# Performance work log

Hardware: AMD Instinct MI355X
Metric: run time of the kernel (lower is better)

Reference implementation:

```python
import jax, jax.numpy as jnp
import numpy as np

B, S, T = 64, 256, 64
E, H = 256, 256
VS, VT = 32000, 32000


def _lstm_cell(x, h, c, Wih, Whh, b):
    # torch gate order: i, f, g, o
    g = x @ Wih.T + h @ Whh.T + b
    i, f, gg, o = jnp.split(g, 4, axis=-1)
    i = jax.nn.sigmoid(i); f = jax.nn.sigmoid(f); o = jax.nn.sigmoid(o)
    gg = jnp.tanh(gg)
    c2 = f * c + i * gg
    h2 = o * jnp.tanh(c2)
    return h2, c2


def _run_lstm(xs, h0, c0, Wih, Whh, b, reverse=False):
    # xs: [S, B, in]
    def step(carry, x):
        h, c = carry
        h2, c2 = _lstm_cell(x, h, c, Wih, Whh, b)
        return (h2, c2), h2
    (hT, cT), ys = jax.lax.scan(step, (h0, c0), xs, reverse=reverse)
    return ys, hT, cT


def setup_inputs():
    key = jax.random.key(0)
    ks = jax.random.split(key, 24)
    sc = 0.05
    rn = lambda k, shp: (jax.random.normal(k, shp, jnp.float32) * sc)
    inp = {
        'src': jax.random.randint(ks[0], (B, S), 0, VS, jnp.int32),
        'tgt_input': jax.random.randint(ks[1], (B, T), 0, VT, jnp.int32),
        'src_emb': rn(ks[2], (VS, E)).at[0].set(0.0),   # padding_idx=0
        'tgt_emb': rn(ks[3], (VT, E)).at[0].set(0.0),
        'enc_f_Wih': rn(ks[4], (4 * H, E)), 'enc_f_Whh': rn(ks[5], (4 * H, H)), 'enc_f_b': rn(ks[6], (4 * H,)),
        'enc_b_Wih': rn(ks[7], (4 * H, E)), 'enc_b_Whh': rn(ks[8], (4 * H, H)), 'enc_b_b': rn(ks[9], (4 * H,)),
        # decoder layer0 input = embed (E) + context (2H)
        'dec0_Wih': rn(ks[10], (4 * H, E + 2 * H)), 'dec0_Whh': rn(ks[11], (4 * H, H)), 'dec0_b': rn(ks[12], (4 * H,)),
        'dec1_Wih': rn(ks[13], (4 * H, H)), 'dec1_Whh': rn(ks[14], (4 * H, H)), 'dec1_b': rn(ks[15], (4 * H,)),
        'attn_W': rn(ks[16], (H, 3 * H)), 'attn_b': rn(ks[17], (H,)),
        'attn_v': jax.random.uniform(ks[18], (H,), jnp.float32),
        'proj_W': rn(ks[19], (VT, H)), 'proj_b': rn(ks[20], (VT,)),
    }
    return inp


def reference(src, tgt_input, src_emb, tgt_emb,
              enc_f_Wih, enc_f_Whh, enc_f_b, enc_b_Wih, enc_b_Whh, enc_b_b,
              dec0_Wih, dec0_Whh, dec0_b, dec1_Wih, dec1_Whh, dec1_b,
              attn_W, attn_b, attn_v, proj_W, proj_b):
    b = src.shape[0]
    zeros = jnp.zeros((b, H), jnp.float32)

    # ---- encoder (1-layer bidirectional LSTM), eval-mode (no dropout) ----
    xs = src_emb[src].transpose(1, 0, 2)  # [S, B, E]
    ys_f, hf, cf = _run_lstm(xs, zeros, zeros, enc_f_Wih, enc_f_Whh, enc_f_b, reverse=False)
    ys_b, hb, cb = _run_lstm(xs, zeros, zeros, enc_b_Wih, enc_b_Whh, enc_b_b, reverse=True)
    enc_out = jnp.concatenate([ys_f, ys_b], axis=-1).transpose(1, 0, 2)  # [B, S, 2H]

    # combined fwd+bwd states, repeated across both decoder layers
    h_init = hf + hb  # [B, H]
    c_init = cf + cb

    # ---- attention precompute: encoder part of attn Linear ----
    Wa_h = attn_W[:, :H]        # applied to decoder hidden
    Wa_e = attn_W[:, H:]        # applied to encoder_outputs
    enc_proj = jnp.einsum('bsd,hd->bsh', enc_out, Wa_e) + attn_b  # [B, S, H]

    # ---- decoder: per-step attention + 2-layer LSTM ----
    tgt_e = tgt_emb[tgt_input].transpose(1, 0, 2)  # [T, B, E]

    def dec_step(carry, emb_t):
        h0, c0, h1, c1 = carry
        # Bahdanau attention on top-layer hidden h1
        energy = jnp.tanh(h1 @ Wa_h.T[..., None, :] if False else
                          jnp.tanh(0.0))  # placeholder never used
        e = jnp.tanh(enc_proj + (h1 @ Wa_h.T)[:, None, :])  # [B, S, H]
        score = jnp.einsum('bsh,h->bs', e, attn_v)
        a = jax.nn.softmax(score, axis=1)
        ctx = jnp.einsum('bs,bsd->bd', a, enc_out)  # [B, 2H]
        x = jnp.concatenate([emb_t, ctx], axis=-1)  # [B, E+2H]
        h0n, c0n = _lstm_cell(x, h0, c0, dec0_Wih, dec0_Whh, dec0_b)
        h1n, c1n = _lstm_cell(h0n, h1, c1, dec1_Wih, dec1_Whh, dec1_b)
        return (h0n, c0n, h1n, c1n), h1n

    _, outs = jax.lax.scan(dec_step, (h_init, c_init, h_init, c_init), tgt_e)
    dec_out = outs.transpose(1, 0, 2)  # [B, T, H]
    logits = dec_out @ proj_W.T + proj_b  # [B, T, VT]
    return logits
```

## Files before the change

### kernel.cpp

```cpp
#include <hip/hip_runtime.h>

typedef unsigned short u16;
typedef unsigned int u32;
typedef unsigned long long u64;
typedef short s8v __attribute__((ext_vector_type(8)));
typedef float f32x4 __attribute__((ext_vector_type(4)));
typedef unsigned short us4 __attribute__((ext_vector_type(4)));

#define MFMA16(a,b,c) __builtin_amdgcn_mfma_f32_16x16x32_bf16(a,b,c,0,0,0)

__device__ __forceinline__ float b2f(u16 u){ union{u32 i; float f;} v; v.i=((u32)u)<<16; return v.f; }
__device__ __forceinline__ u16 f2b(float f){ union{float f; u32 i;} v; v.f=f; u32 r=v.i+0x7FFFu+((v.i>>16)&1u); return (u16)(r>>16); }
__device__ __forceinline__ float sigf(float x){ return 1.f/(1.f+__expf(-x)); }
__device__ __forceinline__ float tanh_(float x){ x=fminf(15.f,fmaxf(-15.f,x)); float e=__expf(2.f*x); return (e-1.f)/(e+1.f); }
__device__ __forceinline__ float tanhs(float x){ float e=__expf(2.f*x); return 1.f - 2.f/(e+1.f); }

union FU { s8v v; us4 h[2]; };

__device__ __forceinline__ us4 ld8_sys(const u16* p){
  u64 v = __hip_atomic_load((const u64*)p, __ATOMIC_RELAXED, __HIP_MEMORY_SCOPE_AGENT);
  union{u64 q; us4 h;} x; x.q=v; return x.h;
}
__device__ __forceinline__ float2 ld8f2(const float* p){
  u64 v = __hip_atomic_load((const u64*)p, __ATOMIC_RELAXED, __HIP_MEMORY_SCOPE_AGENT);
  union{u64 q; float2 f;} x; x.q=v; return x.f;
}
__device__ __forceinline__ void st4_sys(u16* p, u32 v){
  __hip_atomic_store((u32*)p, v, __ATOMIC_RELAXED, __HIP_MEMORY_SCOPE_AGENT);
}
__device__ __forceinline__ void st4f(float* p, float v){
  union{float f; u32 i;} u; u.f=v;
  __hip_atomic_store((u32*)p, u.i, __ATOMIC_RELAXED, __HIP_MEMORY_SCOPE_AGENT);
}
__device__ __forceinline__ void st8_sys(u16* p, us4 v){
  union{us4 h; u64 q;} x; x.h=v;
  __hip_atomic_store((u64*)p, x.q, __ATOMIC_RELAXED, __HIP_MEMORY_SCOPE_AGENT);
}
__device__ __forceinline__ int ldcnt(const int* p){
  return __hip_atomic_load(p, __ATOMIC_RELAXED, __HIP_MEMORY_SCOPE_AGENT);
}
__device__ __forceinline__ void addcnt(int* p){
  __hip_atomic_fetch_add(p, 1, __ATOMIC_RELAXED, __HIP_MEMORY_SCOPE_AGENT);
}

__device__ __forceinline__ s8v gfrag(const u16* rowp, int kbase, int g4){
  FU u; const u16* p = rowp + kbase + 4*g4;
  u.h[0] = *(const us4*)p; u.h[1] = *(const us4*)(p+16);
  return u.v;
}
__device__ __forceinline__ s8v ldsfrag(const u16* lds, int ldk, int row, int kbase, int g4){
  int sw = row&7;
  int g0 = ((kbase+4*g4)>>2)^sw, g1 = ((kbase+16+4*g4)>>2)^sw;
  FU u;
  u.h[0] = *(const us4*)&lds[row*ldk + (g0<<2)];
  u.h[1] = *(const us4*)&lds[row*ldk + (g1<<2)];
  return u.v;
}

__global__ __launch_bounds__(256) void prep_kernel(
    const float* Wihf, const float* Whhf, const float* Wihb, const float* Whhb,
    const float* d0Wih, const float* d0Whh, const float* d1Wih, const float* d1Whh,
    const float* attnW, const float* projW,
    u16* oWihf, u16* oWhhf, u16* oWihb, u16* oWhhb,
    u16* oW0, u16* oW1, u16* oWaH, u16* oWaE, u16* oprojW){
  long long i = (long long)blockIdx.x*256 + threadIdx.x;
  const long long N1 = 262144;
  if (i < N1){ oWihf[i] = f2b(Wihf[i]); return; } i -= N1;
  if (i < N1){ oWhhf[i] = f2b(Whhf[i]); return; } i -= N1;
  if (i < N1){ oWihb[i] = f2b(Wihb[i]); return; } i -= N1;
  if (i < N1){ oWhhb[i] = f2b(Whhb[i]); return; } i -= N1;
  if (i < 1048576){
    int g = (int)(i>>10), k = (int)(i&1023);
    float v = (k<768) ? d0Wih[(size_t)g*768+k] : d0Whh[(size_t)g*256 + (k-768)];
    oW0[i] = f2b(v); return;
  } i -= 1048576;
  if (i < 524288){
    int g = (int)(i>>9), k = (int)(i&511);
    float v = (k<256) ? d1Wih[(size_t)g*256+k] : d1Whh[(size_t)g*256 + (k-256)];
    oW1[i] = f2b(v); return;
  } i -= 524288;
  if (i < 65536){ int n=(int)(i>>8), k=(int)(i&255); oWaH[i] = f2b(attnW[(size_t)n*768+k]); return; } i -= 65536;
  if (i < 131072){ int n=(int)(i>>9), k=(int)(i&511); oWaE[i] = f2b(attnW[(size_t)n*768+256+k]); return; } i -= 131072;
  if (i < 8192000){ oprojW[i] = f2b(projW[i]); return; }
}

__global__ __launch_bounds__(256) void gather_kernel(
    const int* src, const int* tgt, const float* src_emb, const float* tgt_emb,
    u16* xs, u16* temb){
  long long i = (long long)blockIdx.x*256 + threadIdx.x;
  if (i < 4194304){
    int e = (int)(i&255); int sb = (int)(i>>8);
    int s = sb>>6, b = sb&63;
    int idx = src[b*256 + s];
    xs[i] = f2b(src_emb[(size_t)idx*256 + e]);
    return;
  }
  long long j = i - 4194304;
  if (j < 1048576){
    int e = (int)(j&255); int tb = (int)(j>>8);
    int t = tb>>6, b = tb&63;
    int idx = tgt[b*64 + t];
    temb[j] = f2b(tgt_emb[(size_t)idx*256 + e]);
  }
}

template<int K, int OBF>
__global__ __launch_bounds__(256) void gemm64(
    const u16* __restrict__ A, int lda, const u16* __restrict__ Bw, int ldb,
    const float* __restrict__ bias, void* Cout, long long ldc){
  __shared__ u16 Alds[64*K];
  int tid = threadIdx.x;
  long long mt = blockIdx.x, nt = blockIdx.y;
  const int Kc8 = K>>3;
  for (int it = tid; it < 64*Kc8; it += 256){
    int row = it / Kc8, seg = it % Kc8;
    const u16* src = A + (size_t)(mt*64+row)*lda + seg*8;
    us4 a0 = *(const us4*)src, a1 = *(const us4*)(src+4);
    int sw = row&7;
    *(us4*)&Alds[row*K + ((((seg*2  ))^sw)<<2)] = a0;
    *(us4*)&Alds[row*K + ((((seg*2+1))^sw)<<2)] = a1;
  }
  __syncthreads();
  int w = tid>>6, lane = tid&63;
  int l15 = lane&15, g4 = lane>>4;
  int arow = w*16 + l15;
  const int NKT = K>>5;
  s8v af[NKT];
  #pragma unroll
  for (int kt=0; kt<NKT; ++kt) af[kt] = ldsfrag(Alds, K, arow, kt*32, g4);
  f32x4 acc[4];
  #pragma unroll
  for (int nti=0; nti<4; ++nti){
    const u16* brow = Bw + (size_t)(nt*64 + nti*16 + l15)*ldb;
    f32x4 a = {0.f,0.f,0.f,0.f};
    #pragma unroll
    for (int kt=0; kt<NKT; ++kt) a = MFMA16(af[kt], gfrag(brow, kt*32, g4), a);
    acc[nti] = a;
  }
  #pragma unroll
  for (int nti=0; nti<4; ++nti)
    #pragma unroll
    for (int r=0; r<4; ++r){
      long long rowg = mt*64 + w*16 + 4*g4 + r;
      long long colg = nt*64 + nti*16 + l15;
      float v = acc[nti][r] + bias[colg];
      if (OBF) ((u16*)Cout)[rowg*ldc + colg] = f2b(v);
      else     ((float*)Cout)[rowg*ldc + colg] = v;
    }
}

__global__ __launch_bounds__(512,2) void encoder_kernel(
    const u16* __restrict__ XWf, const u16* __restrict__ XWb,
    const u16* __restrict__ Whhf, const u16* __restrict__ Whhb,
    u16* __restrict__ enc_out, float* hTf, float* cTf, float* hTb, float* cTb,
    u16* hx, int* ecnt){
  int bid = blockIdx.x, tid = threadIdx.x;
  int dir = bid&1, bb=(bid>>1)&3, ch=bid>>3;
  const u16* XW  = dir ? XWb : XWf;
  const u16* Whh = dir ? Whhb : Whhf;
  float* hT = dir ? hTb : hTf; float* cT = dir ? cTb : cTf;
  int w = tid>>6, lane = tid&63, l15=lane&15, g4=lane>>4;
  int bg0 = bb*16;
  s8v bwf[4][8];
  #pragma unroll
  for (int i=0;i<4;++i){
    int t4 = w*4+i, q=t4>>3, jt=t4&7;
    const u16* wr = Whh + (size_t)(q*256 + ch*128 + jt*16 + l15)*256;
    #pragma unroll
    for (int kt=0;kt<8;++kt) bwf[i][kt] = gfrag(wr, kt*32, g4);
  }
  int gb = tid>>5, cl = (tid&31)*4;
  float cst[4]={0.f,0.f,0.f,0.f};
  __shared__ u16 hbuf[16*256];
  __shared__ float gacc[512][17];
  for (int i=tid;i<4096;i+=512) hbuf[i]=0;
  __syncthreads();
  int* myc = &ecnt[bid*32];
  int* pc  = &ecnt[(bid^8)*32];
  u16* myhx = hx + (size_t)bid*2*16*128;
  const u16* phx = hx + (size_t)(bid^8)*2*16*128;
  for (int t=0;t<256;++t){
    int s = dir ? 255-t : t;
    us4 xw4[4];
    const u16* xwr = XW + (((size_t)s*64 + bg0 + gb))*1024 + ch*128 + cl;
    #pragma unroll
    for (int qq=0;qq<4;++qq) xw4[qq] = *(const us4*)(xwr + qq*256);
    s8v af[8];
    #pragma unroll
    for (int kt=0;kt<8;++kt) af[kt] = ldsfrag(hbuf, 256, l15, kt*32, g4);
    #pragma unroll
    for (int i=0;i<4;++i){
      f32x4 a={0.f,0.f,0.f,0.f};
      #pragma unroll
      for (int kt=0;kt<8;++kt) a = MFMA16(af[kt], bwf[i][kt], a);
      int t4=w*4+i, q=t4>>3, jt=t4&7;
      #pragma unroll
      for (int r=0;r<4;++r) gacc[q*128 + jt*16 + l15][4*g4+r] = a[r];
    }
    __syncthreads();
    float hvv[4];
    #pragma unroll
    for (int cc=0;cc<4;++cc){
      int clc = cl+cc;
      float gi = gacc[clc][gb]     + b2f(xw4[0][cc]);
      float gf = gacc[128+clc][gb] + b2f(xw4[1][cc]);
      float gg = gacc[256+clc][gb] + b2f(xw4[2][cc]);
      float go = gacc[384+clc][gb] + b2f(xw4[3][cc]);
      float iv=sigf(gi), fv=sigf(gf), gv=tanh_(gg), ov=sigf(go);
      float cn = fv*cst[cc]+iv*gv; cst[cc]=cn;
      hvv[cc] = ov*tanh_(cn);
    }
    us4 hv4;
    #pragma unroll
    for (int cc=0;cc<4;++cc) hv4[cc] = f2b(hvv[cc]);
    *(us4*)&enc_out[(((size_t)(bg0+gb)*256 + s))*512 + dir*256 + ch*128 + cl] = hv4;
    if (t==255){
      #pragma unroll
      for (int cc=0;cc<4;++cc){
        hT[(bg0+gb)*256 + ch*128 + cl+cc] = hvv[cc];
        cT[(bg0+gb)*256 + ch*128 + cl+cc] = cst[cc];
      }
    } else {
      int col = ch*128 + cl;
      *(us4*)&hbuf[gb*256 + ((((col>>2)) ^ (gb&7))<<2)] = hv4;
      st8_sys(myhx + ((size_t)(t&1)*16*128) + gb*128 + cl, hv4);
      asm volatile("s_waitcnt vmcnt(0)" ::: "memory");
      __syncthreads();
      if (tid==0){
        addcnt(myc);
        while (ldcnt(pc) < t+1) __builtin_amdgcn_s_sleep(1);
      }
      __syncthreads();
      int b2 = tid>>5, cl4 = (tid&31)*4;
      us4 pv = ld8_sys(phx + ((size_t)(t&1)*16*128) + b2*128 + cl4);
      int pcol = (1-ch)*128 + cl4;
      *(us4*)&hbuf[b2*256 + ((((pcol>>2)) ^ (b2&7))<<2)] = pv;
      __syncthreads();
    }
  }
}

__global__ __launch_bounds__(256) void init_states(
    const float* hTf, const float* hTb, const float* cTf, const float* cTb,
    float* c0g, float* c1g, u16* h0buf, u16* h1buf){
  int i = blockIdx.x*256 + threadIdx.x;
  float h = hTf[i] + hTb[i];
  float c = cTf[i] + cTb[i];
  c0g[i]=c; c1g[i]=c;
  u16 hb = f2b(h);
  h0buf[16384+i] = hb;
  h1buf[16384+i] = hb;
}

__global__ __launch_bounds__(512,2) void decoder_kernel(
    const u16* __restrict__ epb, const u16* __restrict__ enc, const u16* __restrict__ temb,
    const u16* __restrict__ WaH, const u16* __restrict__ W0, const u16* __restrict__ W1,
    const float* __restrict__ attn_v, const float* __restrict__ b0, const float* __restrict__ b1,
    const float* __restrict__ c0init, const float* __restrict__ c1init,
    u16* h0buf, u16* h1buf, u16* ctxg, float* scoreg, u16* dout, int* dcnt){
  int bid = blockIdx.x, tid = threadIdx.x;
  int c = bid&15, g = bid>>4;
  int w = tid>>6, lane = tid&63, l15 = lane&15, g4 = lane>>4;
  int bg0 = g*8;
  int q = w&3, kh = w>>2;
  const u16* w0r = W0 + (size_t)(q*256 + c*16 + l15)*1024 + kh*512;
  const u16* w1r = W1 + (size_t)(q*256 + c*16 + l15)*512  + kh*256;
  u32 encp[64];
  {
    int dp = lane&15, sq = lane>>4;
    const u16* eb2 = enc + ((size_t)((bg0+w)*256 + sq*64))*512 + c*32 + dp*2;
    #pragma unroll
    for (int sl=0; sl<64; ++sl) encp[sl] = *(const u32*)(eb2 + (size_t)sl*512);
  }
  int cb = tid>>4, ci = tid&15;
  float c0r=0.f, c1r=0.f, bias0[4], bias1[4];
  if (tid<128){
    c0r = c0init[(bg0+cb)*256 + c*16+ci];
    c1r = c1init[(bg0+cb)*256 + c*16+ci];
    #pragma unroll
    for (int qq=0;qq<4;++qq){ bias0[qq]=b0[qq*256 + c*16+ci]; bias1[qq]=b1[qq*256 + c*16+ci]; }
  }
  __shared__ u16 epl[128*264];
  __shared__ u16 x0l[16*1024];
  __shared__ u16 x1l[16*512];
  __shared__ u16 h1l[16*256];
  __shared__ float qls[8][257];
  __shared__ float scls[8][257];
  __shared__ float red[8][16][17];
  __shared__ float vl[256];
  if (tid<256) vl[tid] = attn_v[tid];
  for (int i=tid;i<8192;i+=512) x0l[8192+i]=0;
  for (int i=tid;i<4096;i+=512) x1l[4096+i]=0;
  for (int i=tid;i<2048;i+=512) h1l[2048+i]=0;
  {
    int pr = tid>>2, k2 = tid&3;
    int b2 = pr>>4, sl = pr&15;
    const u16* ep = epb + ((size_t)((bg0+b2)*256 + c*16+sl))*256 + k2*64;
    u16* dst = &epl[(b2*16+sl)*264 + k2*66];
    #pragma unroll
    for (int u2=0; u2<16; ++u2){
      us4 v4 = *(const us4*)(ep + u2*4);
      *(u32*)&dst[u2*4]   = (u32)(u16)v4[0] | ((u32)(u16)v4[1]<<16);
      *(u32*)&dst[u2*4+2] = (u32)(u16)v4[2] | ((u32)(u16)v4[3]<<16);
    }
  }
  __syncthreads();
  int* cnt = &dcnt[g*32];
  int bt = 0;

#define GBAR() do{ bt += 16; \
    asm volatile("s_waitcnt vmcnt(0)" ::: "memory"); \
    __syncthreads(); \
    if (tid==0){ addcnt(cnt); while (ldcnt(cnt) < bt) __builtin_amdgcn_s_sleep(1); } \
    __syncthreads(); }while(0)

  for (int tt=0; tt<64; ++tt){
    int par = tt&1, pp = par^1;
    {
      int b2 = tid>>6, c4 = lane*4;
      us4 hv4 = ld8_sys(h1buf + (size_t)pp*16384 + (bg0+b2)*256 + c4);
      *(us4*)&h1l[b2*256 + ((((c4>>2)) ^ b2)<<2)] = hv4;
      int col = 256 + c4;
      *(us4*)&x1l[b2*512 + ((((col>>2)) ^ b2)<<2)] = hv4;
    }
    __syncthreads();
    #pragma unroll
    for (int t2=0;t2<2;++t2){
      int ct = w*2+t2;
      const u16* br = WaH + (size_t)(ct*16 + l15)*256;
      f32x4 a = {0.f,0.f,0.f,0.f};
      #pragma unroll
      for (int kt=0;kt<8;++kt) a = MFMA16(ldsfrag(h1l,256,l15,kt*32,g4), gfrag(br,kt*32,g4), a);
      #pragma unroll
      for (int r=0;r<4;++r){ int row=4*g4+r; if(row<8) qls[row][ct*16+l15] = a[r]; }
    }
    __syncthreads();
    {
      int pr = tid>>2, k2 = tid&3;
      int b2 = pr>>4, sl = pr&15, s = c*16+sl;
      const u16* base2 = &epl[(b2*16+sl)*264 + k2*66];
      float p = 0.f;
      #pragma unroll 8
      for (int u2=0; u2<32; ++u2){
        u32 e2 = *(const u32*)&base2[u2*2];
        int h = k2*64 + u2*2;
        p += tanhs(b2f((u16)(e2&0xFFFFu)) + qls[b2][h])   * vl[h];
        p += tanhs(b2f((u16)(e2>>16))     + qls[b2][h+1]) * vl[h+1];
      }
      p += __shfl_xor(p,1); p += __shfl_xor(p,2);
      if (k2==0) st4f(scoreg + (size_t)(bg0+b2)*256 + s, p);
    }
    GBAR();
    #pragma unroll
    for (int k=0;k<2;++k){
      int idx = tid + k*512;
      int b2 = idx>>7, s2 = (idx&127)*2;
      float2 f2 = ld8f2(scoreg + (size_t)(bg0+b2)*256 + s2);
      scls[b2][s2] = f2.x; scls[b2][s2+1] = f2.y;
    }
    __syncthreads();
    {
      int b2 = w;
      float a0=scls[b2][lane*4], a1=scls[b2][lane*4+1], a2=scls[b2][lane*4+2], a3=scls[b2][lane*4+3];
      float m = fmaxf(fmaxf(a0,a1),fmaxf(a2,a3));
      #pragma unroll
      for (int o2=32;o2;o2>>=1) m = fmaxf(m, __shfl_xor(m,o2));
      float e0=__expf(a0-m), e1=__expf(a1-m), e2=__expf(a2-m), e3=__expf(a3-m);
      float sm = e0+e1+e2+e3;
      #pragma unroll
      for (int o2=32;o2;o2>>=1) sm += __shfl_xor(sm,o2);
      float inv = 1.f/sm;
      scls[b2][lane*4]=e0*inv; scls[b2][lane*4+1]=e1*inv; scls[b2][lane*4+2]=e2*inv; scls[b2][lane*4+3]=e3*inv;
    }
    __syncthreads();
    {
      int dp = lane&15, sq = lane>>4, b2 = w;
      float cp0=0.f, cp1=0.f;
      #pragma unroll
      for (int sl=0; sl<64; ++sl){
        float wgt = scls[b2][sq*64+sl];
        u32 e2 = encp[sl];
        cp0 += wgt * b2f((u16)(e2&0xFFFFu));
        cp1 += wgt * b2f((u16)(e2>>16));
      }
      cp0 += __shfl_xor(cp0,16); cp0 += __shfl_xor(cp0,32);
      cp1 += __shfl_xor(cp1,16); cp1 += __shfl_xor(cp1,32);
      if (sq==0){
        u32 pk = (u32)f2b(cp0) | ((u32)f2b(cp1)<<16);
        st4_sys(ctxg + (size_t)(bg0+b2)*512 + c*32 + dp*2, pk);
      }
    }
    GBAR();
    {
      int b2 = tid>>6, e4 = lane*4;
      us4 tv = *(const us4*)(temb + ((size_t)tt*64 + bg0 + b2)*256 + e4);
      *(us4*)&x0l[b2*1024 + ((((e4>>2)) ^ b2)<<2)] = tv;
    }
    #pragma unroll
    for (int k=0;k<2;++k){
      int idx = tid + k*512;
      int b2 = idx>>7, c4 = (idx&127)*4;
      us4 cv = ld8_sys(ctxg + (size_t)(bg0+b2)*512 + c4);
      int col = 256 + c4;
      *(us4*)&x0l[b2*1024 + ((((col>>2)) ^ b2)<<2)] = cv;
    }
    {
      int b2 = tid>>6, c4 = lane*4;
      us4 hv4 = ld8_sys(h0buf + (size_t)pp*16384 + (bg0+b2)*256 + c4);
      int col = 768 + c4;
      *(us4*)&x0l[b2*1024 + ((((col>>2)) ^ b2)<<2)] = hv4;
    }
    __syncthreads();
    {
      f32x4 a={0.f,0.f,0.f,0.f};
      #pragma unroll
      for (int kt=0;kt<16;++kt)
        a = MFMA16(ldsfrag(x0l,1024,l15,kh*512+kt*32,g4), gfrag(w0r, kt*32, g4), a);
      #pragma unroll
      for (int r=0;r<4;++r) red[w][4*g4+r][l15] = a[r];
    }
    __syncthreads();
    if (tid<128){
      float gi = red[0][cb][ci]+red[4][cb][ci]+bias0[0];
      float gf = red[1][cb][ci]+red[5][cb][ci]+bias0[1];
      float gg = red[2][cb][ci]+red[6][cb][ci]+bias0[2];
      float go = red[3][cb][ci]+red[7][cb][ci]+bias0[3];
      float iv=sigf(gi), fv=sigf(gf), gv=tanh_(gg), ov=sigf(go);
      float cn = fv*c0r+iv*gv; c0r=cn;
      float hv = ov*tanh_(cn);
      int me=f2b(hv), ot=__shfl_xor(me,1);
      if ((tid&1)==0) st4_sys(h0buf + (size_t)par*16384 + (bg0+cb)*256 + c*16+ci,
                              ((u32)me&0xFFFFu)|((u32)ot<<16));
    }
    GBAR();
    {
      int b2 = tid>>6, c4 = lane*4;
      us4 hv4 = ld8_sys(h0buf + (size_t)par*16384 + (bg0+b2)*256 + c4);
      *(us4*)&x1l[b2*512 + ((((c4>>2)) ^ b2)<<2)] = hv4;
    }
    __syncthreads();
    {
      f32x4 a={0.f,0.f,0.f,0.f};
      #pragma unroll
      for (int kt=0;kt<8;++kt)
        a = MFMA16(ldsfrag(x1l,512,l15,kh*256+kt*32,g4), gfrag(w1r, kt*32, g4), a);
      #pragma unroll
      for (int r=0;r<4;++r) red[w][4*g4+r][l15] = a[r];
    }
    __syncthreads();
    if (tid<128){
      float gi = red[0][cb][ci]+red[4][cb][ci]+bias1[0];
      float gf = red[1][cb][ci]+red[5][cb][ci]+bias1[1];
      float gg = red[2][cb][ci]+red[6][cb][ci]+bias1[2];
      float go = red[3][cb][ci]+red[7][cb][ci]+bias1[3];
      float iv=sigf(gi), fv=sigf(gf), gv=tanh_(gg), ov=sigf(go);
      float cn = fv*c1r+iv*gv; c1r=cn;
      float hv = ov*tanh_(cn);
      int me=f2b(hv), ot=__shfl_xor(me,1);
      if ((tid&1)==0){
        u32 pk = ((u32)me&0xFFFFu)|((u32)ot<<16);
        st4_sys(h1buf + (size_t)par*16384 + (bg0+cb)*256 + c*16+ci, pk);
        *(u32*)&dout[((size_t)(bg0+cb)*64+tt)*256 + c*16+ci] = pk;
      }
    }
    GBAR();
  }
#undef GBAR
}

extern "C" void kernel_launch(void* const* d_in, const int* in_sizes, int n_in,
                              void* d_out, int out_size, void* d_ws, size_t ws_size,
                              hipStream_t stream){
  const int*   src     = (const int*)  d_in[0];
  const int*   tgt     = (const int*)  d_in[1];
  const float* src_emb = (const float*)d_in[2];
  const float* tgt_emb = (const float*)d_in[3];
  const float* encfWih = (const float*)d_in[4];
  const float* encfWhh = (const float*)d_in[5];
  const float* encfb   = (const float*)d_in[6];
  const float* encbWih = (const float*)d_in[7];
  const float* encbWhh = (const float*)d_in[8];
  const float* encbb   = (const float*)d_in[9];
  const float* d0Wih   = (const float*)d_in[10];
  const float* d0Whh   = (const float*)d_in[11];
  const float* d0b     = (const float*)d_in[12];
  const float* d1Wih   = (const float*)d_in[13];
  const float* d1Whh   = (const float*)d_in[14];
  const float* d1b     = (const float*)d_in[15];
  const float* attnW   = (const float*)d_in[16];
  const float* attnb   = (const float*)d_in[17];
  const float* attnv   = (const float*)d_in[18];
  const float* projW   = (const float*)d_in[19];
  const float* projb   = (const float*)d_in[20];

  char* ws = (char*)d_ws;
  size_t off = 0;
  auto alloc = [&](size_t bytes)->char*{ char* p = ws + off; off += (bytes + 255) & ~(size_t)255; return p; };

  int* dcnt     = (int*)alloc(1024);
  int* ecnt     = (int*)alloc(2048);
  u16* xs       = (u16*)alloc(16384ULL*256*2);
  u16* temb     = (u16*)alloc(4096ULL*256*2);
  u16* oWihf    = (u16*)alloc(262144ULL*2);
  u16* oWhhf    = (u16*)alloc(262144ULL*2);
  u16* oWihb    = (u16*)alloc(262144ULL*2);
  u16* oWhhb    = (u16*)alloc(262144ULL*2);
  u16* oW0      = (u16*)alloc(1048576ULL*2);
  u16* oW1      = (u16*)alloc(524288ULL*2);
  u16* oWaH     = (u16*)alloc(65536ULL*2);
  u16* oWaE     = (u16*)alloc(131072ULL*2);
  u16* oprojW   = (u16*)alloc(8192000ULL*2);
  u16* XWf      = (u16*)alloc(16384ULL*1024*2);
  u16* XWb      = (u16*)alloc(16384ULL*1024*2);
  u16* enc      = (u16*)alloc(64ULL*256*512*2);
  u16* epb      = (u16*)alloc(64ULL*256*256*2);
  float* hTf    = (float*)alloc(16384ULL*4);
  float* cTf    = (float*)alloc(16384ULL*4);
  float* hTb    = (float*)alloc(16384ULL*4);
  float* cTb    = (float*)alloc(16384ULL*4);
  float* c0g    = (float*)alloc(16384ULL*4);
  float* c1g    = (float*)alloc(16384ULL*4);
  u16* h0buf    = (u16*)alloc(2ULL*16384*2);
  u16* h1buf    = (u16*)alloc(2ULL*16384*2);
  u16* ctxg     = (u16*)alloc(64ULL*512*2);
  float* scoreg = (float*)alloc(16384ULL*4);
  u16* hx       = (u16*)alloc(16ULL*2*16*128*2);
  u16* dout     = (u16*)alloc(4096ULL*256*2);
  if (off > ws_size) return;

  hipMemsetAsync(dcnt, 0, 1024, stream);
  hipMemsetAsync(ecnt, 0, 2048, stream);

  prep_kernel<<<43008, 256, 0, stream>>>(encfWih, encfWhh, encbWih, encbWhh,
      d0Wih, d0Whh, d1Wih, d1Whh, attnW, projW,
      oWihf, oWhhf, oWihb, oWhhb, oW0, oW1, oWaH, oWaE, oprojW);

  gather_kernel<<<20480, 256, 0, stream>>>(src, tgt, src_emb, tgt_emb, xs, temb);

  gemm64<256,1><<<dim3(256,16), 256, 0, stream>>>(xs, 256, oWihf, 256, encfb, XWf, 1024);
  gemm64<256,1><<<dim3(256,16), 256, 0, stream>>>(xs, 256, oWihb, 256, encbb, XWb, 1024);

  encoder_kernel<<<16, 512, 0, stream>>>(XWf, XWb, oWhhf, oWhhb, enc, hTf, cTf, hTb, cTb, hx, ecnt);

  gemm64<512,1><<<dim3(256,4), 256, 0, stream>>>(enc, 512, oWaE, 512, attnb, epb, 256);

  init_states<<<64, 256, 0, stream>>>(hTf, hTb, cTf, cTb, c0g, c1g, h0buf, h1buf);

  decoder_kernel<<<128, 512, 0, stream>>>(epb, enc, temb, oWaH, oW0, oW1,
      attnv, d0b, d1b, c0g, c1g, h0buf, h1buf, ctxg, scoreg, dout, dcnt);

  gemm64<256,0><<<dim3(64,500), 256, 0, stream>>>(dout, 256, oprojW, 256, projb, (float*)d_out, 32000);
}
```

Before: 4.728 ms.

## Use per-block flag barrier in decoder and stream encoder Whh from memory

The decoder's group barrier switches from a shared atomic counter (one fetch_add per block, then polling) to per-block flags on separate cache lines. Each block stores its epoch, and one wavefront polls all 16 flags in parallel and min-reduces them with shuffles, which removes atomic contention on a single counter. Separately, the encoder no longer keeps the Whh fragments in registers; it reloads them from global or L2 memory each timestep. This frees a large number of registers but adds memory traffic on the serial recurrence path.

```diff
diff --git a/kernel.cpp b/kernel.cpp
--- a/kernel.cpp
+++ b/kernel.cpp
@@ -38,6 +38,9 @@
 }
 __device__ __forceinline__ int ldcnt(const int* p){
   return __hip_atomic_load(p, __ATOMIC_RELAXED, __HIP_MEMORY_SCOPE_AGENT);
+}
+__device__ __forceinline__ void stcnt(int* p, int v){
+  __hip_atomic_store(p, v, __ATOMIC_RELAXED, __HIP_MEMORY_SCOPE_AGENT);
 }
 __device__ __forceinline__ void addcnt(int* p){
   __hip_atomic_fetch_add(p, 1, __ATOMIC_RELAXED, __HIP_MEMORY_SCOPE_AGENT);
@@ -161,13 +164,11 @@
   float* hT = dir ? hTb : hTf; float* cT = dir ? cTb : cTf;
   int w = tid>>6, lane = tid&63, l15=lane&15, g4=lane>>4;
   int bg0 = bb*16;
-  s8v bwf[4][8];
+  const u16* wrp[4];
   #pragma unroll
   for (int i=0;i<4;++i){
     int t4 = w*4+i, q=t4>>3, jt=t4&7;
-    const u16* wr = Whh + (size_t)(q*256 + ch*128 + jt*16 + l15)*256;
-    #pragma unroll
-    for (int kt=0;kt<8;++kt) bwf[i][kt] = gfrag(wr, kt*32, g4);
+    wrp[i] = Whh + (size_t)(q*256 + ch*128 + jt*16 + l15)*256;
   }
   int gb = tid>>5, cl = (tid&31)*4;
   float cst[4]={0.f,0.f,0.f,0.f};
@@ -192,7 +193,7 @@
     for (int i=0;i<4;++i){
       f32x4 a={0.f,0.f,0.f,0.f};
       #pragma unroll
-      for (int kt=0;kt<8;++kt) a = MFMA16(af[kt], bwf[i][kt], a);
+      for (int kt=0;kt<8;++kt) a = MFMA16(af[kt], gfrag(wrp[i], kt*32, g4), a);
       int t4=w*4+i, q=t4>>3, jt=t4&7;
       #pragma unroll
       for (int r=0;r<4;++r) gacc[q*128 + jt*16 + l15][4*g4+r] = a[r];
@@ -257,7 +258,7 @@
     const u16* __restrict__ WaH, const u16* __restrict__ W0, const u16* __restrict__ W1,
     const float* __restrict__ attn_v, const float* __restrict__ b0, const float* __restrict__ b1,
     const float* __restrict__ c0init, const float* __restrict__ c1init,
-    u16* h0buf, u16* h1buf, u16* ctxg, float* scoreg, u16* dout, int* dcnt){
+    u16* h0buf, u16* h1buf, u16* ctxg, float* scoreg, u16* dout, int* dflag){
   int bid = blockIdx.x, tid = threadIdx.x;
   int c = bid&15, g = bid>>4;
   int w = tid>>6, lane = tid&63, l15 = lane&15, g4 = lane>>4;
@@ -305,13 +306,25 @@
     }
   }
   __syncthreads();
-  int* cnt = &dcnt[g*32];
+  int* myflag = &dflag[(g*16 + c)*64];
+  int* gflags = &dflag[g*16*64];
   int bt = 0;
 
-#define GBAR() do{ bt += 16; \
+#define GBAR() do{ bt += 1; \
     asm volatile("s_waitcnt vmcnt(0)" ::: "memory"); \
     __syncthreads(); \
-    if (tid==0){ addcnt(cnt); while (ldcnt(cnt) < bt) __builtin_amdgcn_s_sleep(1); } \
+    if (tid==0) stcnt(myflag, bt); \
+    if (tid<64){ \
+      int v_; \
+      do{ __builtin_amdgcn_s_sleep(1); \
+          v_ = ldcnt(&gflags[(lane&15)*64]); \
+          int m_; \
+          m_ = __shfl_xor(v_,1); v_ = v_<m_?v_:m_; \
+          m_ = __shfl_xor(v_,2); v_ = v_<m_?v_:m_; \
+          m_ = __shfl_xor(v_,4); v_ = v_<m_?v_:m_; \
+          m_ = __shfl_xor(v_,8); v_ = v_<m_?v_:m_; \
+      } while (v_ < bt); \
+    } \
     __syncthreads(); }while(0)
 
   for (int tt=0; tt<64; ++tt){
@@ -497,7 +510,7 @@
   size_t off = 0;
   auto alloc = [&](size_t bytes)->char*{ char* p = ws + off; off += (bytes + 255) & ~(size_t)255; return p; };
 
-  int* dcnt     = (int*)alloc(1024);
+  int* dflag    = (int*)alloc(32768);
   int* ecnt     = (int*)alloc(2048);
   u16* xs       = (u16*)alloc(16384ULL*256*2);
   u16* temb     = (u16*)alloc(4096ULL*256*2);
@@ -528,7 +541,7 @@
   u16* dout     = (u16*)alloc(4096ULL*256*2);
   if (off > ws_size) return;
 
-  hipMemsetAsync(dcnt, 0, 1024, stream);
+  hipMemsetAsync(dflag, 0, 32768, stream);
   hipMemsetAsync(ecnt, 0, 2048, stream);
 
   prep_kernel<<<43008, 256, 0, stream>>>(encfWih, encfWhh, encbWih, encbWhh,
@@ -547,7 +560,7 @@
   init_states<<<64, 256, 0, stream>>>(hTf, hTb, cTf, cTb, c0g, c1g, h0buf, h1buf);
 
   decoder_kernel<<<128, 512, 0, stream>>>(epb, enc, temb, oWaH, oW0, oW1,
-      attnv, d0b, d1b, c0g, c1g, h0buf, h1buf, ctxg, scoreg, dout, dcnt);
+      attnv, d0b, d1b, c0g, c1g, h0buf, h1buf, ctxg, scoreg, dout, dflag);
 
   gemm64<256,0><<<dim3(64,500), 256, 0, stream>>>(dout, 256, oprojW, 256, projb, (float*)d_out, 32000);
 }
```

After: 4.717 ms. About the same (-0.2%).

## Decoder: one block per batch row, drop grid barriers; encoder streams Whh

Applied to the files above, without the earlier changes.

The decoder is restructured from 128 cooperating blocks that synchronised through global-memory counters into 64 independent 1024-thread blocks, each owning a single batch row for all timesteps. This removes the per-step grid barriers and the global round trips for scores, context and hidden states. The cost is much worse MFMA utilisation: only one row of each 16-row tile is non-zero, so every block re-reads the full W0/W1/WaH weights from global or L2 on each step. The encoder also stops keeping Whh fragments in registers and reloads them from global memory every timestep, which lowers register pressure but adds memory traffic.

```diff
diff --git a/kernel.cpp b/kernel.cpp
--- a/kernel.cpp
+++ b/kernel.cpp
@@ -20,17 +20,6 @@
 __device__ __forceinline__ us4 ld8_sys(const u16* p){
   u64 v = __hip_atomic_load((const u64*)p, __ATOMIC_RELAXED, __HIP_MEMORY_SCOPE_AGENT);
   union{u64 q; us4 h;} x; x.q=v; return x.h;
-}
-__device__ __forceinline__ float2 ld8f2(const float* p){
-  u64 v = __hip_atomic_load((const u64*)p, __ATOMIC_RELAXED, __HIP_MEMORY_SCOPE_AGENT);
-  union{u64 q; float2 f;} x; x.q=v; return x.f;
-}
-__device__ __forceinline__ void st4_sys(u16* p, u32 v){
-  __hip_atomic_store((u32*)p, v, __ATOMIC_RELAXED, __HIP_MEMORY_SCOPE_AGENT);
-}
-__device__ __forceinline__ void st4f(float* p, float v){
-  union{float f; u32 i;} u; u.f=v;
-  __hip_atomic_store((u32*)p, u.i, __ATOMIC_RELAXED, __HIP_MEMORY_SCOPE_AGENT);
 }
 __device__ __forceinline__ void st8_sys(u16* p, us4 v){
   union{us4 h; u64 q;} x; x.h=v;
@@ -161,13 +150,11 @@
   float* hT = dir ? hTb : hTf; float* cT = dir ? cTb : cTf;
   int w = tid>>6, lane = tid&63, l15=lane&15, g4=lane>>4;
   int bg0 = bb*16;
-  s8v bwf[4][8];
+  const u16* wrp[4];
   #pragma unroll
   for (int i=0;i<4;++i){
     int t4 = w*4+i, q=t4>>3, jt=t4&7;
-    const u16* wr = Whh + (size_t)(q*256 + ch*128 + jt*16 + l15)*256;
-    #pragma unroll
-    for (int kt=0;kt<8;++kt) bwf[i][kt] = gfrag(wr, kt*32, g4);
+    wrp[i] = Whh + (size_t)(q*256 + ch*128 + jt*16 + l15)*256;
   }
   int gb = tid>>5, cl = (tid&31)*4;
   float cst[4]={0.f,0.f,0.f,0.f};
@@ -192,7 +179,7 @@
     for (int i=0;i<4;++i){
       f32x4 a={0.f,0.f,0.f,0.f};
       #pragma unroll
-      for (int kt=0;kt<8;++kt) a = MFMA16(af[kt], bwf[i][kt], a);
+      for (int kt=0;kt<8;++kt) a = MFMA16(af[kt], gfrag(wrp[i], kt*32, g4), a);
       int t4=w*4+i, q=t4>>3, jt=t4&7;
       #pragma unroll
       for (int r=0;r<4;++r) gacc[q*128 + jt*16 + l15][4*g4+r] = a[r];
@@ -252,51 +239,31 @@
   h1buf[16384+i] = hb;
 }
 
-__global__ __launch_bounds__(512,2) void decoder_kernel(
+__global__ __launch_bounds__(1024,1) void decoder_kernel(
     const u16* __restrict__ epb, const u16* __restrict__ enc, const u16* __restrict__ temb,
     const u16* __restrict__ WaH, const u16* __restrict__ W0, const u16* __restrict__ W1,
     const float* __restrict__ attn_v, const float* __restrict__ b0, const float* __restrict__ b1,
     const float* __restrict__ c0init, const float* __restrict__ c1init,
-    u16* h0buf, u16* h1buf, u16* ctxg, float* scoreg, u16* dout, int* dcnt){
-  int bid = blockIdx.x, tid = threadIdx.x;
-  int c = bid&15, g = bid>>4;
-  int w = tid>>6, lane = tid&63, l15 = lane&15, g4 = lane>>4;
-  int bg0 = g*8;
-  int q = w&3, kh = w>>2;
-  const u16* w0r = W0 + (size_t)(q*256 + c*16 + l15)*1024 + kh*512;
-  const u16* w1r = W1 + (size_t)(q*256 + c*16 + l15)*512  + kh*256;
-  u32 encp[64];
+    const u16* __restrict__ hinit, u16* __restrict__ dout){
+  int b = blockIdx.x, tid = threadIdx.x;
+  int wv = tid>>6, lane = tid&63, l15 = lane&15, g4 = lane>>4;
+  __shared__ u16 epl[256*264];
+  __shared__ float part[4][512];
+  __shared__ float qls[256];
+  __shared__ float scs[256];
+  __shared__ float af2[256];
+  __shared__ float vl[256];
+  __shared__ float gacc[1024];
+  __shared__ float c0l[256];
+  __shared__ float c1l[256];
+  __shared__ u16 x0l[1024];
+  __shared__ u16 x1l[512];
+  __shared__ u16 h0l[256];
+  __shared__ u16 h1l[256];
   {
-    int dp = lane&15, sq = lane>>4;
-    const u16* eb2 = enc + ((size_t)((bg0+w)*256 + sq*64))*512 + c*32 + dp*2;
-    #pragma unroll
-    for (int sl=0; sl<64; ++sl) encp[sl] = *(const u32*)(eb2 + (size_t)sl*512);
-  }
-  int cb = tid>>4, ci = tid&15;
-  float c0r=0.f, c1r=0.f, bias0[4], bias1[4];
-  if (tid<128){
-    c0r = c0init[(bg0+cb)*256 + c*16+ci];
-    c1r = c1init[(bg0+cb)*256 + c*16+ci];
-    #pragma unroll
-    for (int qq=0;qq<4;++qq){ bias0[qq]=b0[qq*256 + c*16+ci]; bias1[qq]=b1[qq*256 + c*16+ci]; }
-  }
-  __shared__ u16 epl[128*264];
-  __shared__ u16 x0l[16*1024];
-  __shared__ u16 x1l[16*512];
-  __shared__ u16 h1l[16*256];
-  __shared__ float qls[8][257];
-  __shared__ float scls[8][257];
-  __shared__ float red[8][16][17];
-  __shared__ float vl[256];
-  if (tid<256) vl[tid] = attn_v[tid];
-  for (int i=tid;i<8192;i+=512) x0l[8192+i]=0;
-  for (int i=tid;i<4096;i+=512) x1l[4096+i]=0;
-  for (int i=tid;i<2048;i+=512) h1l[2048+i]=0;
-  {
-    int pr = tid>>2, k2 = tid&3;
-    int b2 = pr>>4, sl = pr&15;
-    const u16* ep = epb + ((size_t)((bg0+b2)*256 + c*16+sl))*256 + k2*64;
-    u16* dst = &epl[(b2*16+sl)*264 + k2*66];
+    int s = tid>>2, k2 = tid&3;
+    const u16* ep = epb + ((size_t)(b*256 + s))*256 + k2*64;
+    u16* dst = &epl[s*264 + k2*66];
     #pragma unroll
     for (int u2=0; u2<16; ++u2){
       us4 v4 = *(const us4*)(ep + u2*4);
@@ -304,64 +271,48 @@
       *(u32*)&dst[u2*4+2] = (u32)(u16)v4[2] | ((u32)(u16)v4[3]<<16);
     }
   }
+  if (tid<256){
+    vl[tid] = attn_v[tid];
+    u16 h = hinit[b*256+tid];
+    h1l[tid] = h; h0l[tid] = h;
+    c0l[tid] = c0init[b*256+tid];
+    c1l[tid] = c1init[b*256+tid];
+  }
   __syncthreads();
-  int* cnt = &dcnt[g*32];
-  int bt = 0;
-
-#define GBAR() do{ bt += 16; \
-    asm volatile("s_waitcnt vmcnt(0)" ::: "memory"); \
-    __syncthreads(); \
-    if (tid==0){ addcnt(cnt); while (ldcnt(cnt) < bt) __builtin_amdgcn_s_sleep(1); } \
-    __syncthreads(); }while(0)
-
+  const s8v zf = {0,0,0,0,0,0,0,0};
   for (int tt=0; tt<64; ++tt){
-    int par = tt&1, pp = par^1;
     {
-      int b2 = tid>>6, c4 = lane*4;
-      us4 hv4 = ld8_sys(h1buf + (size_t)pp*16384 + (bg0+b2)*256 + c4);
-      *(us4*)&h1l[b2*256 + ((((c4>>2)) ^ b2)<<2)] = hv4;
-      int col = 256 + c4;
-      *(us4*)&x1l[b2*512 + ((((col>>2)) ^ b2)<<2)] = hv4;
-    }
-    __syncthreads();
-    #pragma unroll
-    for (int t2=0;t2<2;++t2){
-      int ct = w*2+t2;
-      const u16* br = WaH + (size_t)(ct*16 + l15)*256;
-      f32x4 a = {0.f,0.f,0.f,0.f};
-      #pragma unroll
-      for (int kt=0;kt<8;++kt) a = MFMA16(ldsfrag(h1l,256,l15,kt*32,g4), gfrag(br,kt*32,g4), a);
-      #pragma unroll
-      for (int r=0;r<4;++r){ int row=4*g4+r; if(row<8) qls[row][ct*16+l15] = a[r]; }
+      int h = tid>>2, k2 = tid&3;
+      const u16* wr = WaH + (size_t)h*256 + k2*64;
+      float qv = 0.f;
+      #pragma unroll 4
+      for (int u2=0; u2<16; ++u2){
+        us4 w4 = *(const us4*)(wr + u2*4);
+        int k = k2*64 + u2*4;
+        qv += b2f(w4[0])*b2f(h1l[k])   + b2f(w4[1])*b2f(h1l[k+1])
+            + b2f(w4[2])*b2f(h1l[k+2]) + b2f(w4[3])*b2f(h1l[k+3]);
+      }
+      qv += __shfl_xor(qv,1); qv += __shfl_xor(qv,2);
+      if (k2==0) qls[h] = qv;
     }
     __syncthreads();
     {
-      int pr = tid>>2, k2 = tid&3;
-      int b2 = pr>>4, sl = pr&15, s = c*16+sl;
-      const u16* base2 = &epl[(b2*16+sl)*264 + k2*66];
+      int s = tid>>2, k2 = tid&3;
+      const u16* base2 = &epl[s*264 + k2*66];
       float p = 0.f;
       #pragma unroll 8
       for (int u2=0; u2<32; ++u2){
         u32 e2 = *(const u32*)&base2[u2*2];
         int h = k2*64 + u2*2;
-        p += tanhs(b2f((u16)(e2&0xFFFFu)) + qls[b2][h])   * vl[h];
-        p += tanhs(b2f((u16)(e2>>16))     + qls[b2][h+1]) * vl[h+1];
+        p += tanhs(b2f((u16)(e2&0xFFFFu)) + qls[h])   * vl[h];
+        p += tanhs(b2f((u16)(e2>>16))     + qls[h+1]) * vl[h+1];
       }
       p += __shfl_xor(p,1); p += __shfl_xor(p,2);
-      if (k2==0) st4f(scoreg + (size_t)(bg0+b2)*256 + s, p);
-    }
-    GBAR();
-    #pragma unroll
-    for (int k=0;k<2;++k){
-      int idx = tid + k*512;
-      int b2 = idx>>7, s2 = (idx&127)*2;
-      float2 f2 = ld8f2(scoreg + (size_t)(bg0+b2)*256 + s2);
-      scls[b2][s2] = f2.x; scls[b2][s2+1] = f2.y;
-    }
-    __syncthreads();
-    {
-      int b2 = w;
-      float a0=scls[b2][lane*4], a1=scls[b2][lane*4+1], a2=scls[b2][lane*4+2], a3=scls[b2][lane*4+3];
+      if (k2==0) scs[s] = p;
+    }
+    __syncthreads();
+    if (wv==0){
+      float a0=scs[lane*4],a1=scs[lane*4+1],a2=scs[lane*4+2],a3=scs[lane*4+3];
       float m = fmaxf(fmaxf(a0,a1),fmaxf(a2,a3));
       #pragma unroll
       for (int o2=32;o2;o2>>=1) m = fmaxf(m, __shfl_xor(m,o2));
@@ -370,102 +321,106 @@
       #pragma unroll
       for (int o2=32;o2;o2>>=1) sm += __shfl_xor(sm,o2);
       float inv = 1.f/sm;
-      scls[b2][lane*4]=e0*inv; scls[b2][lane*4+1]=e1*inv; scls[b2][lane*4+2]=e2*inv; scls[b2][lane*4+3]=e3*inv;
+      af2[lane*4]=e0*inv; af2[lane*4+1]=e1*inv; af2[lane*4+2]=e2*inv; af2[lane*4+3]=e3*inv;
     }
     __syncthreads();
     {
-      int dp = lane&15, sq = lane>>4, b2 = w;
+      int soff = tid>>8, dp = tid&255;
+      const u16* ebase = enc + ((size_t)b*256)*512 + dp*2;
       float cp0=0.f, cp1=0.f;
-      #pragma unroll
-      for (int sl=0; sl<64; ++sl){
-        float wgt = scls[b2][sq*64+sl];
-        u32 e2 = encp[sl];
+      #pragma unroll 8
+      for (int ck=0; ck<64; ++ck){
+        int s = ck*4 + soff;
+        u32 e2 = *(const u32*)(ebase + (size_t)s*512);
+        float wgt = af2[s];
         cp0 += wgt * b2f((u16)(e2&0xFFFFu));
         cp1 += wgt * b2f((u16)(e2>>16));
       }
-      cp0 += __shfl_xor(cp0,16); cp0 += __shfl_xor(cp0,32);
-      cp1 += __shfl_xor(cp1,16); cp1 += __shfl_xor(cp1,32);
-      if (sq==0){
-        u32 pk = (u32)f2b(cp0) | ((u32)f2b(cp1)<<16);
-        st4_sys(ctxg + (size_t)(bg0+b2)*512 + c*32 + dp*2, pk);
-      }
-    }
-    GBAR();
+      part[soff][dp*2] = cp0; part[soff][dp*2+1] = cp1;
+    }
+    __syncthreads();
+    if (tid<512){
+      float cx = part[0][tid]+part[1][tid]+part[2][tid]+part[3][tid];
+      x0l[256+tid] = f2b(cx);
+    } else if (tid<768){
+      int j = tid-512;
+      x0l[j] = temb[((size_t)tt*64 + b)*256 + j];
+    } else {
+      int j = tid-768;
+      x0l[768+j] = h0l[j];
+    }
+    __syncthreads();
     {
-      int b2 = tid>>6, e4 = lane*4;
-      us4 tv = *(const us4*)(temb + ((size_t)tt*64 + bg0 + b2)*256 + e4);
-      *(us4*)&x0l[b2*1024 + ((((e4>>2)) ^ b2)<<2)] = tv;
-    }
-    #pragma unroll
-    for (int k=0;k<2;++k){
-      int idx = tid + k*512;
-      int b2 = idx>>7, c4 = (idx&127)*4;
-      us4 cv = ld8_sys(ctxg + (size_t)(bg0+b2)*512 + c4);
-      int col = 256 + c4;
-      *(us4*)&x0l[b2*1024 + ((((col>>2)) ^ b2)<<2)] = cv;
-    }
+      f32x4 acc0={0.f,0.f,0.f,0.f},acc1={0.f,0.f,0.f,0.f},acc2={0.f,0.f,0.f,0.f},acc3={0.f,0.f,0.f,0.f};
+      const u16* wbase = W0 + (size_t)(wv*64 + l15)*1024;
+      for (int kt=0; kt<32; ++kt){
+        s8v af = zf;
+        if (l15==0){
+          FU u; u.h[0] = *(const us4*)&x0l[kt*32+4*g4]; u.h[1] = *(const us4*)&x0l[kt*32+4*g4+16];
+          af = u.v;
+        }
+        acc0 = MFMA16(af, gfrag(wbase,           kt*32, g4), acc0);
+        acc1 = MFMA16(af, gfrag(wbase + 16*1024, kt*32, g4), acc1);
+        acc2 = MFMA16(af, gfrag(wbase + 32*1024, kt*32, g4), acc2);
+        acc3 = MFMA16(af, gfrag(wbase + 48*1024, kt*32, g4), acc3);
+      }
+      if (g4==0){
+        gacc[wv*64 + l15]      = acc0[0];
+        gacc[wv*64 + 16 + l15] = acc1[0];
+        gacc[wv*64 + 32 + l15] = acc2[0];
+        gacc[wv*64 + 48 + l15] = acc3[0];
+      }
+    }
+    __syncthreads();
+    if (tid<256){
+      float iv = sigf(gacc[tid]      + b0[tid]);
+      float fv = sigf(gacc[256+tid]  + b0[256+tid]);
+      float gv = tanh_(gacc[512+tid] + b0[512+tid]);
+      float ov = sigf(gacc[768+tid]  + b0[768+tid]);
+      float cn = fv*c0l[tid] + iv*gv; c0l[tid] = cn;
+      float hv = ov*tanh_(cn);
+      u16 hb = f2b(hv);
+      h0l[tid] = hb;
+      x1l[tid] = hb;
+    } else if (tid<512){
+      x1l[tid] = h1l[tid-256];
+    }
+    __syncthreads();
     {
-      int b2 = tid>>6, c4 = lane*4;
-      us4 hv4 = ld8_sys(h0buf + (size_t)pp*16384 + (bg0+b2)*256 + c4);
-      int col = 768 + c4;
-      *(us4*)&x0l[b2*1024 + ((((col>>2)) ^ b2)<<2)] = hv4;
-    }
-    __syncthreads();
-    {
-      f32x4 a={0.f,0.f,0.f,0.f};
-      #pragma unroll
-      for (int kt=0;kt<16;++kt)
-        a = MFMA16(ldsfrag(x0l,1024,l15,kh*512+kt*32,g4), gfrag(w0r, kt*32, g4), a);
-      #pragma unroll
-      for (int r=0;r<4;++r) red[w][4*g4+r][l15] = a[r];
-    }
-    __syncthreads();
-    if (tid<128){
-      float gi = red[0][cb][ci]+red[4][cb][ci]+bias0[0];
-      float gf = red[1][cb][ci]+red[5][cb][ci]+bias0[1];
-      float gg = red[2][cb][ci]+red[6][cb][ci]+bias0[2];
-      float go = red[3][cb][ci]+red[7][cb][ci]+bias0[3];
-      float iv=sigf(gi), fv=sigf(gf), gv=tanh_(gg), ov=sigf(go);
-      float cn = fv*c0r+iv*gv; c0r=cn;
+      f32x4 acc0={0.f,0.f,0.f,0.f},acc1={0.f,0.f,0.f,0.f},acc2={0.f,0.f,0.f,0.f},acc3={0.f,0.f,0.f,0.f};
+      const u16* wbase = W1 + (size_t)(wv*64 + l15)*512;
+      for (int kt=0; kt<16; ++kt){
+        s8v af = zf;
+        if (l15==0){
+          FU u; u.h[0] = *(const us4*)&x1l[kt*32+4*g4]; u.h[1] = *(const us4*)&x1l[kt*32+4*g4+16];
+          af = u.v;
+        }
+        acc0 = MFMA16(af, gfrag(wbase,          kt*32, g4), acc0);
+        acc1 = MFMA16(af, gfrag(wbase + 16*512, kt*32, g4), acc1);
+        acc2 = MFMA16(af, gfrag(wbase + 32*512, kt*32, g4), acc2);
+        acc3 = MFMA16(af, gfrag(wbase + 48*512, kt*32, g4), acc3);
+      }
+      if (g4==0){
+        gacc[wv*64 + l15]      = acc0[0];
+        gacc[wv*64 + 16 + l15] = acc1[0];
+        gacc[wv*64 + 32 + l15] = acc2[0];
+        gacc[wv*64 + 48 + l15] = acc3[0];
+      }
+    }
+    __syncthreads();
+    if (tid<256){
+      float iv = sigf(gacc[tid]      + b1[tid]);
+      float fv = sigf(gacc[256+tid]  + b1[256+tid]);
+      float gv = tanh_(gacc[512+tid] + b1[512+tid]);
+      float ov = sigf(gacc[768+tid]  + b1[768+tid]);
+      float cn = fv*c1l[tid] + iv*gv; c1l[tid] = cn;
       float hv = ov*tanh_(cn);
-      int me=f2b(hv), ot=__shfl_xor(me,1);
-      if ((tid&1)==0) st4_sys(h0buf + (size_t)par*16384 + (bg0+cb)*256 + c*16+ci,
-                              ((u32)me&0xFFFFu)|((u32)ot<<16));
-    }
-    GBAR();
-    {
-      int b2 = tid>>6, c4 = lane*4;
-      us4 hv4 = ld8_sys(h0buf + (size_t)par*16384 + (bg0+b2)*256 + c4);
-      *(us4*)&x1l[b2*512 + ((((c4>>2)) ^ b2)<<2)] = hv4;
-    }
-    __syncthreads();
-    {
-      f32x4 a={0.f,0.f,0.f,0.f};
-      #pragma unroll
-      for (int kt=0;kt<8;++kt)
-        a = MFMA16(ldsfrag(x1l,512,l15,kh*256+kt*32,g4), gfrag(w1r, kt*32, g4), a);
-      #pragma unroll
-      for (int r=0;r<4;++r) red[w][4*g4+r][l15] = a[r];
-    }
-    __syncthreads();
-    if (tid<128){
-      float gi = red[0][cb][ci]+red[4][cb][ci]+bias1[0];
-      float gf = red[1][cb][ci]+red[5][cb][ci]+bias1[1];
-      float gg = red[2][cb][ci]+red[6][cb][ci]+bias1[2];
-      float go = red[3][cb][ci]+red[7][cb][ci]+bias1[3];
-      float iv=sigf(gi), fv=sigf(gf), gv=tanh_(gg), ov=sigf(go);
-      float cn = fv*c1r+iv*gv; c1r=cn;
-      float hv = ov*tanh_(cn);
-      int me=f2b(hv), ot=__shfl_xor(me,1);
-      if ((tid&1)==0){
-        u32 pk = ((u32)me&0xFFFFu)|((u32)ot<<16);
-        st4_sys(h1buf + (size_t)par*16384 + (bg0+cb)*256 + c*16+ci, pk);
-        *(u32*)&dout[((size_t)(bg0+cb)*64+tt)*256 + c*16+ci] = pk;
-      }
-    }
-    GBAR();
-  }
-#undef GBAR
+      u16 hb = f2b(hv);
+      h1l[tid] = hb;
+      dout[((size_t)b*64 + tt)*256 + tid] = hb;
+    }
+    __syncthreads();
+  }
 }
 
 extern "C" void kernel_launch(void* const* d_in, const int* in_sizes, int n_in,
@@ -497,7 +452,6 @@
   size_t off = 0;
   auto alloc = [&](size_t bytes)->char*{ char* p = ws + off; off += (bytes + 255) & ~(size_t)255; return p; };
 
-  int* dcnt     = (int*)alloc(1024);
   int* ecnt     = (int*)alloc(2048);
   u16* xs       = (u16*)alloc(16384ULL*256*2);
   u16* temb     = (u16*)alloc(4096ULL*256*2);
@@ -522,13 +476,10 @@
   float* c1g    = (float*)alloc(16384ULL*4);
   u16* h0buf    = (u16*)alloc(2ULL*16384*2);
   u16* h1buf    = (u16*)alloc(2ULL*16384*2);
-  u16* ctxg     = (u16*)alloc(64ULL*512*2);
-  float* scoreg = (float*)alloc(16384ULL*4);
   u16* hx       = (u16*)alloc(16ULL*2*16*128*2);
   u16* dout     = (u16*)alloc(4096ULL*256*2);
   if (off > ws_size) return;
 
-  hipMemsetAsync(dcnt, 0, 1024, stream);
   hipMemsetAsync(ecnt, 0, 2048, stream);
 
   prep_kernel<<<43008, 256, 0, stream>>>(encfWih, encfWhh, encbWih, encbWhh,
@@ -546,8 +497,8 @@
 
   init_states<<<64, 256, 0, stream>>>(hTf, hTb, cTf, cTb, c0g, c1g, h0buf, h1buf);
 
-  decoder_kernel<<<128, 512, 0, stream>>>(epb, enc, temb, oWaH, oW0, oW1,
-      attnv, d0b, d1b, c0g, c1g, h0buf, h1buf, ctxg, scoreg, dout, dcnt);
+  decoder_kernel<<<64, 1024, 0, stream>>>(epb, enc, temb, oWaH, oW0, oW1,
+      attnv, d0b, d1b, c0g, c1g, h0buf + 16384, dout);
 
   gemm64<256,0><<<dim3(64,500), 256, 0, stream>>>(dout, 256, oprojW, 256, projb, (float*)d_out, 32000);
 }
```

After: 9.475 ms. 100% more time.
